# Performance work log

Measured on AMD Instinct MI355X. Metric: run time of the kernel, lower is better.

The kernel has to match this reference:

```python
import jax, jax.numpy as jnp
import numpy as np

EPS = 1e-12

def setup_inputs() -> dict:
    key = jax.random.key(0)
    k1, k2, k3, k4, k5 = jax.random.split(key, 5)
    n, C, B = 8, 1024, 2048
    X = jax.random.normal(k1, (n, C, B), dtype=jnp.float32)
    # xavier_uniform bound for square [C, C] weight
    bound = float(np.sqrt(6.0 / (C + C)))
    Wk_w = jax.random.uniform(k2, (C, C), dtype=jnp.float32, minval=-bound, maxval=bound)
    Wq_w = jax.random.uniform(k3, (C, C), dtype=jnp.float32, minval=-bound, maxval=bound)
    # nn.Linear default bias init: U(-1/sqrt(C), 1/sqrt(C))
    bb = 1.0 / float(np.sqrt(C))
    Wk_b = jax.random.uniform(k4, (C,), dtype=jnp.float32, minval=-bb, maxval=bb)
    Wq_b = jax.random.uniform(k5, (C,), dtype=jnp.float32, minval=-bb, maxval=bb)
    return {"X": X, "Wk_w": Wk_w, "Wk_b": Wk_b, "Wq_w": Wq_w, "Wq_b": Wq_b}

def reference(X, Wk_w, Wk_b, Wq_w, Wq_b):
    # X: [n, C, B]; weights: [C, C]; biases: [C]
    K = jnp.einsum('oc,ncb->nob', Wk_w, X) + Wk_b[:, None]   # [n, C, B]
    Q = jnp.einsum('oc,ncb->nob', Wq_w, X) + Wq_b[:, None]   # [n, C, B]
    DK2 = jnp.sum(K * K, axis=1)                              # [n, B]
    DQ2 = jnp.sum(Q * Q, axis=1)                              # [n, B]
    DQK = jnp.sqrt(jnp.maximum(DQ2[:, :, None] * DK2[:, None, :], EPS))  # [n, B, B]
    Y = jnp.einsum('ncb,nck->nbk', Q, K) / DQK                # [n, B, B] cosine-like scores
    SM = jax.nn.softmax(Y, axis=1)                            # softmax over query axis (dim=1)
    Z = jnp.einsum('ncb,nbk->nck', X, SM)                     # [n, C, B]
    return Z
```

## Files before the change

### kernel.cpp

```cpp
#include <hip/hip_runtime.h>
#include <hip/hip_bf16.h>

typedef __bf16 v8bf __attribute__((ext_vector_type(8)));
typedef __bf16 v4bf __attribute__((ext_vector_type(4)));
typedef float  v4f  __attribute__((ext_vector_type(4)));

#define AS1 __attribute__((address_space(1)))
#define AS3 __attribute__((address_space(3)))

static __device__ __forceinline__ void gload_lds16(const void* g, void* l) {
  __builtin_amdgcn_global_load_lds((const AS1 void*)g, (AS3 void*)l, 16, 0, 0);
}

__global__ __launch_bounds__(256)
void cvt_bf16(const float* __restrict__ in, __bf16* __restrict__ out, long n) {
  const long i = ((long)blockIdx.x * 256 + threadIdx.x) * 4;
  if (i >= n) return;
  v4f v = *(const v4f*)&in[i];
  v4bf o;
#pragma unroll
  for (int u = 0; u < 4; ++u) o[u] = (__bf16)v[u];
  *(v4bf*)&out[i] = o;
}

__global__ __launch_bounds__(256)
void zero_f32(float* __restrict__ p, long n) {
  const long i = ((long)blockIdx.x * 256 + threadIdx.x) * 4;
  if (i >= n) return;
  *(v4f*)&p[i] = v4f{0.f, 0.f, 0.f, 0.f};
}

__global__ __launch_bounds__(256)
void cvt_transpose(const float* __restrict__ X, __bf16* __restrict__ XT) {
  __shared__ float t[64][65];
  const int b0 = blockIdx.x * 64, c0 = blockIdx.y * 64;
  const long n = blockIdx.z;
  const float* Xp = X + n * (1024L * 2048);
  __bf16* Tp = XT + n * (2048L * 1024);
  const int tid = threadIdx.x;
  const int r16 = tid >> 4, c4 = (tid & 15) * 4;
#pragma unroll
  for (int it = 0; it < 4; ++it) {
    const int r = r16 + it * 16;
    *(v4f*)&t[r][c4] = *(const v4f*)&Xp[(long)(c0 + r) * 2048 + b0 + c4];
  }
  __syncthreads();
  const int rb8 = tid >> 3, c8 = (tid & 7) * 8;
#pragma unroll
  for (int it = 0; it < 2; ++it) {
    const int rb = rb8 + it * 32;
    v8bf o;
#pragma unroll
    for (int u = 0; u < 8; ++u) o[u] = (__bf16)t[c8 + u][rb];
    *(v8bf*)&Tp[(long)(b0 + rb) * 1024 + c0 + c8] = o;
  }
}

#define BAR __builtin_amdgcn_s_barrier()
#define LGKM0 do { asm volatile("s_waitcnt lgkmcnt(0)" ::: "memory"); \
                   __builtin_amdgcn_sched_barrier(0); } while (0)
#define VMW(N) do { asm volatile("s_waitcnt vmcnt(" #N ")" ::: "memory"); \
                    __builtin_amdgcn_sched_barrier(0); } while (0)
#define MM(HM, HN) do { \
  __builtin_amdgcn_s_setprio(1); \
  _Pragma("unroll") for (int ks = 0; ks < 2; ++ks) \
  _Pragma("unroll") for (int u = 0; u < 2; ++u) \
  _Pragma("unroll") for (int j = 0; j < 4; ++j) \
    acc[2 * (HM) + u][4 * (HN) + j] = __builtin_amdgcn_mfma_f32_16x16x32_bf16( \
        bfr[j][ks], af[u][ks], acc[2 * (HM) + u][4 * (HN) + j], 0, 0, 0); \
  __builtin_amdgcn_s_setprio(0); } while (0)

template<int KD, int EPI, typename OT>
__global__ __launch_bounds__(512, 2)
void gemm256(const __bf16* __restrict__ Abase, const __bf16* __restrict__ Bbase,
             OT* __restrict__ Obase, const __bf16* __restrict__ bias,
             float* __restrict__ dk2, const float* __restrict__ dq2,
             long sA, long sB, long sO) {
  __shared__ __align__(128) __bf16 lds[65536];

  const int tid = threadIdx.x;
  const int wave = tid >> 6, lane = tid & 63;
  const int qr = wave >> 1, qc = wave & 1;
  const int fr = lane & 15, q = lane >> 4;
  const int f7 = fr & 7;

  const int gx = gridDim.x, gy = gridDim.y;
  int id = blockIdx.x + gx * (blockIdx.y + gy * blockIdx.z);
  const int chunk = (gx * gy * gridDim.z) >> 3;
  id = (id & 7) * chunk + (id >> 3);
  const int bx = id % gx;
  const int rem = id / gx;
  const int by = rem % gy;
  const long z = rem / gy;

  const int n0 = bx * 256, m0 = by * 256;
  const __bf16* A = Abase + z * sA + (long)m0 * KD;
  const __bf16* B = Bbase + z * sB + (long)n0 * KD;

  const int lrow = wave * 16 + (lane >> 3);
  const int lchunk = ((lane & 7) ^ (lane >> 3)) << 3;
  const __bf16* Alane = A + (long)lrow * KD + lchunk;
  const __bf16* Blane = B + (long)lrow * KD + lchunk;
  const int dbase = wave * 1024;

  auto stage = [&](int kt, int isB, int half) {
    const __bf16* gp = (isB ? Blane : Alane) + (long)(half * 128) * KD + kt * 64;
    __bf16* dp = lds + (kt & 1) * 32768 + isB * 16384 + half * 8192 + dbase;
    gload_lds16(gp, dp);
    gload_lds16(gp + (long)8 * KD, dp + 512);
  };

  v4f acc[4][8];
#pragma unroll
  for (int i = 0; i < 4; ++i)
#pragma unroll
    for (int j = 0; j < 8; ++j) acc[i][j] = {0.f, 0.f, 0.f, 0.f};

  v8bf af[2][2], bfr[4][2];
  auto readA = [&](const __bf16* sa, int hm) {
#pragma unroll
    for (int u = 0; u < 2; ++u) {
      const int rb = (hm * 128 + qr * 32 + u * 16 + fr) * 64;
      af[u][0] = *(const v8bf*)&sa[rb + ((q ^ f7) << 3)];
      af[u][1] = *(const v8bf*)&sa[rb + (((q | 4) ^ f7) << 3)];
    }
  };
  auto readB = [&](const __bf16* sb, int hn) {
#pragma unroll
    for (int j = 0; j < 4; ++j) {
      const int rb = (hn * 128 + qc * 64 + j * 16 + fr) * 64;
      bfr[j][0] = *(const v8bf*)&sb[rb + ((q ^ f7) << 3)];
      bfr[j][1] = *(const v8bf*)&sb[rb + (((q | 4) ^ f7) << 3)];
    }
  };

  constexpr int NT = KD / 64;
  constexpr int NI = NT / 2;
  __bf16* s0 = lds;
  __bf16* s1 = lds + 32768;

  stage(0, 0, 0); stage(0, 1, 0); stage(0, 0, 1); stage(0, 1, 1);
  stage(1, 1, 0); stage(1, 0, 1); stage(1, 1, 1);
  VMW(6); BAR;

#pragma unroll 1
  for (int m = 0; m < NI; ++m) {
    const bool nl = (m != NI - 1);
    const int t1 = 2 * m + 1, t2 = 2 * m + 2, t3 = 2 * m + 3;
    readA(s0, 0); readB(s0 + 16384, 0);
    stage(t1, 0, 0);
    LGKM0; BAR; MM(0, 0);
    readA(s0, 1);
    if (nl) stage(t2, 1, 0);
    LGKM0; BAR; MM(1, 0);
    readB(s0 + 16384, 1);
    if (nl) stage(t2, 0, 1);
    LGKM0; BAR; MM(1, 1);
    readA(s0, 0);
    if (nl) stage(t2, 1, 1);
    LGKM0;
    if (nl) { VMW(6); } else { VMW(0); }
    BAR; MM(0, 1);
    readA(s1, 0); readB(s1 + 16384, 0);
    if (nl) stage(t2, 0, 0);
    LGKM0; BAR; MM(0, 0);
    readA(s1, 1);
    if (nl) stage(t3, 1, 0);
    LGKM0; BAR; MM(1, 0);
    readB(s1 + 16384, 1);
    if (nl) stage(t3, 0, 1);
    LGKM0; BAR; MM(1, 1);
    readA(s1, 0);
    if (nl) stage(t3, 1, 1);
    LGKM0;
    if (nl) { VMW(6); } else { VMW(0); }
    BAR; MM(0, 1);
  }

  OT* O = Obase + z * sO;
  const int ldo = gx * 256;
#pragma unroll
  for (int ai = 0; ai < 4; ++ai) {
    const int row = m0 + (ai >> 1) * 128 + qr * 32 + (ai & 1) * 16 + fr;
    float rk = 0.f;
    if (EPI == 1) rk = dk2[z * 2048 + row];
    float rs = 0.f;
#pragma unroll
    for (int bj = 0; bj < 8; ++bj) {
      const int colb = n0 + (bj >> 2) * 128 + qc * 64 + (bj & 3) * 16 + q * 4;
      float cv[4];
      if (EPI == 0) {
        v4bf bb = *(const v4bf*)&bias[colb];
#pragma unroll
        for (int r = 0; r < 4; ++r) cv[r] = (float)bb[r];
      }
      if (EPI == 1) {
        v4f dd = *(const v4f*)&dq2[z * 2048 + colb];
#pragma unroll
        for (int r = 0; r < 4; ++r) cv[r] = dd[r];
      }
      float vv[4];
#pragma unroll
      for (int r = 0; r < 4; ++r) {
        float v = acc[ai][bj][r];
        if (EPI == 0) {
          v = fminf(fmaxf(v + cv[r], -32.f), 32.f);
          rs += v * v;
        }
        if (EPI == 1) {
          v *= rsqrtf(fmaxf(rk * cv[r], 1e-12f));
          v = fminf(fmaxf(v, -4.f), 4.f);
        }
        if (EPI == 2) v = fminf(fmaxf(v, -1.f), 1.f);
        vv[r] = v;
      }
      if (sizeof(OT) == 2) {
        v4bf o;
#pragma unroll
        for (int r = 0; r < 4; ++r) o[r] = (__bf16)vv[r];
        *(v4bf*)&O[(long)row * ldo + colb] = o;
      } else {
        v4f o;
#pragma unroll
        for (int r = 0; r < 4; ++r) o[r] = vv[r];
        *(v4f*)&O[(long)row * ldo + colb] = o;
      }
    }
    if (EPI == 0) {
      rs += __shfl_xor(rs, 16);
      rs += __shfl_xor(rs, 32);
      if (q == 0) atomicAdd(&dk2[z * 2048 + row], rs);
    }
  }
}

__global__ __launch_bounds__(256)
void softmax_rows(__bf16* __restrict__ Y) {
  const int tid = threadIdx.x;
  const long row = (long)blockIdx.y * gridDim.x + blockIdx.x;
  __bf16* p = Y + row * 2048;
  v8bf v = *(const v8bf*)&p[tid * 8];
  float f[8];
  float s = 0.f;
#pragma unroll
  for (int u = 0; u < 8; ++u) { f[u] = __expf((float)v[u]); s += f[u]; }
#pragma unroll
  for (int off = 32; off > 0; off >>= 1) s += __shfl_down(s, off);
  __shared__ float red[4];
  __shared__ float stot;
  if ((tid & 63) == 0) red[tid >> 6] = s;
  __syncthreads();
  if (tid == 0) stot = 1.f / (red[0] + red[1] + red[2] + red[3]);
  __syncthreads();
  const float inv = stot;
  v8bf o;
#pragma unroll
  for (int u = 0; u < 8; ++u) o[u] = (__bf16)(f[u] * inv);
  *(v8bf*)&p[tid * 8] = o;
}

extern "C" void kernel_launch(void* const* d_in, const int* in_sizes, int n_in,
                              void* d_out, int out_size, void* d_ws, size_t ws_size,
                              hipStream_t stream) {
  const float* X    = (const float*)d_in[0];
  const float* Wk_w = (const float*)d_in[1];
  const float* Wk_b = (const float*)d_in[2];
  const float* Wq_w = (const float*)d_in[3];
  const float* Wq_b = (const float*)d_in[4];
  float* out = (float*)d_out;

  char* ws = (char*)d_ws;
  __bf16* XT  = (__bf16*)(ws);
  __bf16* Xbf = (__bf16*)(ws);
  __bf16* YT  = (__bf16*)(ws + 33554432L);
  char* aux   = ws + 100663296L;
  float*  DK2   = (float*)(aux);
  float*  DQ2   = (float*)(aux + 65536L);
  __bf16* Wk_bf = (__bf16*)(aux + 131072L);
  __bf16* Wq_bf = (__bf16*)(aux + 131072L + 2097152L);
  __bf16* bk_bf = (__bf16*)(aux + 131072L + 4194304L);
  __bf16* bq_bf = (__bf16*)(aux + 131072L + 4196352L);
  __bf16* KT = (__bf16*)d_out;
  __bf16* QT = (__bf16*)((char*)d_out + 33554432L);

  cvt_bf16<<<1024, 256, 0, stream>>>(Wk_w, Wk_bf, 1048576L);
  cvt_bf16<<<1024, 256, 0, stream>>>(Wq_w, Wq_bf, 1048576L);
  cvt_bf16<<<1, 256, 0, stream>>>(Wk_b, bk_bf, 1024L);
  cvt_bf16<<<1, 256, 0, stream>>>(Wq_b, bq_bf, 1024L);
  zero_f32<<<32, 256, 0, stream>>>(DK2, 32768L);
  cvt_transpose<<<dim3(32, 16, 8), 256, 0, stream>>>(X, XT);
  gemm256<1024, 0, __bf16><<<dim3(4, 8, 8), 512, 0, stream>>>(
      XT, Wk_bf, KT, bk_bf, DK2, nullptr, 2048L * 1024, 0L, 2048L * 1024);
  gemm256<1024, 0, __bf16><<<dim3(4, 8, 8), 512, 0, stream>>>(
      XT, Wq_bf, QT, bq_bf, DQ2, nullptr, 2048L * 1024, 0L, 2048L * 1024);
  cvt_bf16<<<16384, 256, 0, stream>>>(X, Xbf, 16777216L);
  gemm256<1024, 1, __bf16><<<dim3(8, 8, 8), 512, 0, stream>>>(
      KT, QT, YT, nullptr, DK2, DQ2, 2048L * 1024, 2048L * 1024, 2048L * 2048);
  softmax_rows<<<dim3(2048, 8), 256, 0, stream>>>(YT);
  gemm256<2048, 2, float><<<dim3(8, 4, 8), 512, 0, stream>>>(
      Xbf, YT, out, nullptr, nullptr, nullptr, 1024L * 2048, 2048L * 2048, 1024L * 2048);
}
```

Before: 366.7 us.

## Switch GEMM to 32x32x16 MFMA with four-stage K=32 LDS pipeline

Replaces the 16x16x32 MFMA tiling with 32x32x16 bf16 MFMAs, so each wave holds 2x4 blocks of 32x32 accumulators instead of 4x8 blocks of 16x16. The LDS staging moves from two 64-wide K buffers, filled in half-tiles, to four 32-wide K buffers. Each stage prefetches three tiles ahead, with one readAB and one MMALL per K step. Larger MFMAs cut LDS fragment reads per FLOP and issue overhead. The deeper pipeline and new swizzle change barrier counts and bank-conflict behaviour, and could hurt if the swizzle conflicts or the extra barriers stall.

Measured after the change: 404.6 us. 10.3% more time.

```diff
diff --git a/kernel.cpp b/kernel.cpp
--- a/kernel.cpp
+++ b/kernel.cpp
@@ -4,6 +4,7 @@
 typedef __bf16 v8bf __attribute__((ext_vector_type(8)));
 typedef __bf16 v4bf __attribute__((ext_vector_type(4)));
 typedef float  v4f  __attribute__((ext_vector_type(4)));
+typedef float  f32x16 __attribute__((ext_vector_type(16)));
 
 #define AS1 __attribute__((address_space(1)))
 #define AS3 __attribute__((address_space(3)))
@@ -61,13 +62,13 @@
                    __builtin_amdgcn_sched_barrier(0); } while (0)
 #define VMW(N) do { asm volatile("s_waitcnt vmcnt(" #N ")" ::: "memory"); \
                     __builtin_amdgcn_sched_barrier(0); } while (0)
-#define MM(HM, HN) do { \
+#define MMALL do { \
   __builtin_amdgcn_s_setprio(1); \
-  _Pragma("unroll") for (int ks = 0; ks < 2; ++ks) \
-  _Pragma("unroll") for (int u = 0; u < 2; ++u) \
-  _Pragma("unroll") for (int j = 0; j < 4; ++j) \
-    acc[2 * (HM) + u][4 * (HN) + j] = __builtin_amdgcn_mfma_f32_16x16x32_bf16( \
-        bfr[j][ks], af[u][ks], acc[2 * (HM) + u][4 * (HN) + j], 0, 0, 0); \
+  _Pragma("unroll") for (int s = 0; s < 2; ++s) \
+  _Pragma("unroll") for (int h = 0; h < 2; ++h) \
+  _Pragma("unroll") for (int nb = 0; nb < 4; ++nb) \
+    acc[h][nb] = __builtin_amdgcn_mfma_f32_32x32x16_bf16( \
+        bf_[nb][s], af[h][s], acc[h][nb], 0, 0, 0); \
   __builtin_amdgcn_s_setprio(0); } while (0)
 
 template<int KD, int EPI, typename OT>
@@ -81,13 +82,13 @@
   const int tid = threadIdx.x;
   const int wave = tid >> 6, lane = tid & 63;
   const int qr = wave >> 1, qc = wave & 1;
-  const int fr = lane & 15, q = lane >> 4;
-  const int f7 = fr & 7;
+  const int l31 = lane & 31, hi = lane >> 5;
+  const int sw = (l31 >> 1) & 3;
 
   const int gx = gridDim.x, gy = gridDim.y;
   int id = blockIdx.x + gx * (blockIdx.y + gy * blockIdx.z);
-  const int chunk = (gx * gy * gridDim.z) >> 3;
-  id = (id & 7) * chunk + (id >> 3);
+  const int chunk8 = (gx * gy * gridDim.z) >> 3;
+  id = (id & 7) * chunk8 + (id >> 3);
   const int bx = id % gx;
   const int rem = id / gx;
   const int by = rem % gy;
@@ -97,139 +98,127 @@
   const __bf16* A = Abase + z * sA + (long)m0 * KD;
   const __bf16* B = Bbase + z * sB + (long)n0 * KD;
 
-  const int lrow = wave * 16 + (lane >> 3);
-  const int lchunk = ((lane & 7) ^ (lane >> 3)) << 3;
-  const __bf16* Alane = A + (long)lrow * KD + lchunk;
-  const __bf16* Blane = B + (long)lrow * KD + lchunk;
-  const int dbase = wave * 1024;
-
-  auto stage = [&](int kt, int isB, int half) {
-    const __bf16* gp = (isB ? Blane : Alane) + (long)(half * 128) * KD + kt * 64;
-    __bf16* dp = lds + (kt & 1) * 32768 + isB * 16384 + half * 8192 + dbase;
-    gload_lds16(gp, dp);
-    gload_lds16(gp + (long)8 * KD, dp + 512);
+  const int srow = lane >> 2;
+  const int schunk = ((lane & 3) ^ ((lane >> 3) & 3)) << 3;
+  const __bf16* Alane = A + (long)(wave * 32 + srow) * KD + schunk;
+  const __bf16* Blane = B + (long)(wave * 32 + srow) * KD + schunk;
+  const int dst = wave * 1024;
+
+  auto stage = [&](int kt) {
+    const int bb = (kt & 3) * 16384;
+    const __bf16* ga = Alane + kt * 32;
+    gload_lds16(ga, lds + bb + dst);
+    gload_lds16(ga + (long)16 * KD, lds + bb + dst + 512);
+    const __bf16* gb = Blane + kt * 32;
+    gload_lds16(gb, lds + bb + 8192 + dst);
+    gload_lds16(gb + (long)16 * KD, lds + bb + 8192 + dst + 512);
   };
 
-  v4f acc[4][8];
-#pragma unroll
-  for (int i = 0; i < 4; ++i)
-#pragma unroll
-    for (int j = 0; j < 8; ++j) acc[i][j] = {0.f, 0.f, 0.f, 0.f};
-
-  v8bf af[2][2], bfr[4][2];
-  auto readA = [&](const __bf16* sa, int hm) {
-#pragma unroll
-    for (int u = 0; u < 2; ++u) {
-      const int rb = (hm * 128 + qr * 32 + u * 16 + fr) * 64;
-      af[u][0] = *(const v8bf*)&sa[rb + ((q ^ f7) << 3)];
-      af[u][1] = *(const v8bf*)&sa[rb + (((q | 4) ^ f7) << 3)];
-    }
+  f32x16 acc[2][4];
+#pragma unroll
+  for (int h = 0; h < 2; ++h)
+#pragma unroll
+    for (int nb = 0; nb < 4; ++nb)
+#pragma unroll
+      for (int r = 0; r < 16; ++r) acc[h][nb][r] = 0.f;
+
+  v8bf af[2][2], bf_[4][2];
+  auto readAB = [&](int buf) {
+    const __bf16* sa = lds + buf * 16384;
+    const __bf16* sb = sa + 8192;
+#pragma unroll
+    for (int h = 0; h < 2; ++h)
+#pragma unroll
+      for (int s = 0; s < 2; ++s)
+        af[h][s] = *(const v8bf*)
+            &sa[(h * 128 + qr * 32 + l31) * 32 + (((2 * s + hi) ^ sw) << 3)];
+#pragma unroll
+    for (int nb = 0; nb < 4; ++nb)
+#pragma unroll
+      for (int s = 0; s < 2; ++s)
+        bf_[nb][s] = *(const v8bf*)
+            &sb[((nb >> 1) * 128 + qc * 64 + (nb & 1) * 32 + l31) * 32 +
+                (((2 * s + hi) ^ sw) << 3)];
   };
-  auto readB = [&](const __bf16* sb, int hn) {
-#pragma unroll
-    for (int j = 0; j < 4; ++j) {
-      const int rb = (hn * 128 + qc * 64 + j * 16 + fr) * 64;
-      bfr[j][0] = *(const v8bf*)&sb[rb + ((q ^ f7) << 3)];
-      bfr[j][1] = *(const v8bf*)&sb[rb + (((q | 4) ^ f7) << 3)];
-    }
-  };
-
-  constexpr int NT = KD / 64;
-  constexpr int NI = NT / 2;
-  __bf16* s0 = lds;
-  __bf16* s1 = lds + 32768;
-
-  stage(0, 0, 0); stage(0, 1, 0); stage(0, 0, 1); stage(0, 1, 1);
-  stage(1, 1, 0); stage(1, 0, 1); stage(1, 1, 1);
-  VMW(6); BAR;
+
+  constexpr int NT = KD / 32;
+  constexpr int NI = NT / 8;
+
+  stage(0); stage(1); stage(2);
+  VMW(8); BAR;
 
 #pragma unroll 1
   for (int m = 0; m < NI; ++m) {
+    const int T = m * 8;
     const bool nl = (m != NI - 1);
-    const int t1 = 2 * m + 1, t2 = 2 * m + 2, t3 = 2 * m + 3;
-    readA(s0, 0); readB(s0 + 16384, 0);
-    stage(t1, 0, 0);
-    LGKM0; BAR; MM(0, 0);
-    readA(s0, 1);
-    if (nl) stage(t2, 1, 0);
-    LGKM0; BAR; MM(1, 0);
-    readB(s0 + 16384, 1);
-    if (nl) stage(t2, 0, 1);
-    LGKM0; BAR; MM(1, 1);
-    readA(s0, 0);
-    if (nl) stage(t2, 1, 1);
-    LGKM0;
-    if (nl) { VMW(6); } else { VMW(0); }
-    BAR; MM(0, 1);
-    readA(s1, 0); readB(s1 + 16384, 0);
-    if (nl) stage(t2, 0, 0);
-    LGKM0; BAR; MM(0, 0);
-    readA(s1, 1);
-    if (nl) stage(t3, 1, 0);
-    LGKM0; BAR; MM(1, 0);
-    readB(s1 + 16384, 1);
-    if (nl) stage(t3, 0, 1);
-    LGKM0; BAR; MM(1, 1);
-    readA(s1, 0);
-    if (nl) stage(t3, 1, 1);
-    LGKM0;
-    if (nl) { VMW(6); } else { VMW(0); }
-    BAR; MM(0, 1);
+#pragma unroll
+    for (int q = 0; q < 8; ++q) {
+      readAB(q & 3);
+      if (nl || q <= 4) stage(T + q + 3);
+      BAR; LGKM0;
+      MMALL;
+      if (nl || q <= 4) { VMW(8); }
+      else if (q == 5)  { VMW(4); }
+      else if (q == 6)  { VMW(0); }
+      if (nl || q != 7) BAR;
+    }
   }
 
   OT* O = Obase + z * sO;
   const int ldo = gx * 256;
 #pragma unroll
-  for (int ai = 0; ai < 4; ++ai) {
-    const int row = m0 + (ai >> 1) * 128 + qr * 32 + (ai & 1) * 16 + fr;
-    float rk = 0.f;
+  for (int h = 0; h < 2; ++h) {
+    const int row = m0 + h * 128 + qr * 32 + l31;
+    float rk = 0.f, rs = 0.f;
     if (EPI == 1) rk = dk2[z * 2048 + row];
-    float rs = 0.f;
-#pragma unroll
-    for (int bj = 0; bj < 8; ++bj) {
-      const int colb = n0 + (bj >> 2) * 128 + qc * 64 + (bj & 3) * 16 + q * 4;
-      float cv[4];
-      if (EPI == 0) {
-        v4bf bb = *(const v4bf*)&bias[colb];
-#pragma unroll
-        for (int r = 0; r < 4; ++r) cv[r] = (float)bb[r];
-      }
-      if (EPI == 1) {
-        v4f dd = *(const v4f*)&dq2[z * 2048 + colb];
-#pragma unroll
-        for (int r = 0; r < 4; ++r) cv[r] = dd[r];
-      }
-      float vv[4];
-#pragma unroll
-      for (int r = 0; r < 4; ++r) {
-        float v = acc[ai][bj][r];
+#pragma unroll
+    for (int nb = 0; nb < 4; ++nb) {
+#pragma unroll
+      for (int t = 0; t < 4; ++t) {
+        const int colb = n0 + (nb >> 1) * 128 + qc * 64 + (nb & 1) * 32 +
+                         t * 8 + hi * 4;
+        float cv[4];
         if (EPI == 0) {
-          v = fminf(fmaxf(v + cv[r], -32.f), 32.f);
-          rs += v * v;
+          v4bf bb = *(const v4bf*)&bias[colb];
+#pragma unroll
+          for (int r = 0; r < 4; ++r) cv[r] = (float)bb[r];
         }
         if (EPI == 1) {
-          v *= rsqrtf(fmaxf(rk * cv[r], 1e-12f));
-          v = fminf(fmaxf(v, -4.f), 4.f);
-        }
-        if (EPI == 2) v = fminf(fmaxf(v, -1.f), 1.f);
-        vv[r] = v;
-      }
-      if (sizeof(OT) == 2) {
-        v4bf o;
-#pragma unroll
-        for (int r = 0; r < 4; ++r) o[r] = (__bf16)vv[r];
-        *(v4bf*)&O[(long)row * ldo + colb] = o;
-      } else {
-        v4f o;
-#pragma unroll
-        for (int r = 0; r < 4; ++r) o[r] = vv[r];
-        *(v4f*)&O[(long)row * ldo + colb] = o;
+          v4f dd = *(const v4f*)&dq2[z * 2048 + colb];
+#pragma unroll
+          for (int r = 0; r < 4; ++r) cv[r] = dd[r];
+        }
+        float vv[4];
+#pragma unroll
+        for (int r = 0; r < 4; ++r) {
+          float v = acc[h][nb][t * 4 + r];
+          if (EPI == 0) {
+            v = fminf(fmaxf(v + cv[r], -32.f), 32.f);
+            rs += v * v;
+          }
+          if (EPI == 1) {
+            v *= rsqrtf(fmaxf(rk * cv[r], 1e-12f));
+            v = fminf(fmaxf(v, -4.f), 4.f);
+          }
+          if (EPI == 2) v = fminf(fmaxf(v, -1.f), 1.f);
+          vv[r] = v;
+        }
+        if (sizeof(OT) == 2) {
+          v4bf o;
+#pragma unroll
+          for (int r = 0; r < 4; ++r) o[r] = (__bf16)vv[r];
+          *(v4bf*)&O[(long)row * ldo + colb] = o;
+        } else {
+          v4f o;
+#pragma unroll
+          for (int r = 0; r < 4; ++r) o[r] = vv[r];
+          *(v4f*)&O[(long)row * ldo + colb] = o;
+        }
       }
     }
     if (EPI == 0) {
-      rs += __shfl_xor(rs, 16);
       rs += __shfl_xor(rs, 32);
-      if (q == 0) atomicAdd(&dk2[z * 2048 + row], rs);
+      if (hi == 0) atomicAdd(&dk2[z * 2048 + row], rs);
     }
   }
 }
```

## Switch GEMM inner loop to 32x32x16 bf16 MFMA with separate A fragment buffers

Applied to the files above, without the earlier changes.

Replaces the 16x16x32 MFMA tiling with 32x32x16 MFMA instructions, reshaping the accumulators into four 16-float vectors per half and rewriting the LDS fragment reads and epilogue indexing to match. Keeping two A fragment buffers (af0/af1) lets the fourth sub-step reuse the already-loaded A fragment, dropping one LDS re-read and one lgkm wait per half-iteration. Larger MFMA tiles cut the instruction count and the LDS traffic per FLOP, at the cost of a different register footprint and a changed LDS access pattern that could conflict with the swizzle.

New measurement: 396.9 us. +8.2%, slower.

```diff
diff --git a/kernel.cpp b/kernel.cpp
--- a/kernel.cpp
+++ b/kernel.cpp
@@ -4,6 +4,7 @@
 typedef __bf16 v8bf __attribute__((ext_vector_type(8)));
 typedef __bf16 v4bf __attribute__((ext_vector_type(4)));
 typedef float  v4f  __attribute__((ext_vector_type(4)));
+typedef float  f32x16 __attribute__((ext_vector_type(16)));
 
 #define AS1 __attribute__((address_space(1)))
 #define AS3 __attribute__((address_space(3)))
@@ -61,13 +62,12 @@
                    __builtin_amdgcn_sched_barrier(0); } while (0)
 #define VMW(N) do { asm volatile("s_waitcnt vmcnt(" #N ")" ::: "memory"); \
                     __builtin_amdgcn_sched_barrier(0); } while (0)
-#define MM(HM, HN) do { \
+#define MM(AF, HM, NP) do { \
   __builtin_amdgcn_s_setprio(1); \
-  _Pragma("unroll") for (int ks = 0; ks < 2; ++ks) \
-  _Pragma("unroll") for (int u = 0; u < 2; ++u) \
-  _Pragma("unroll") for (int j = 0; j < 4; ++j) \
-    acc[2 * (HM) + u][4 * (HN) + j] = __builtin_amdgcn_mfma_f32_16x16x32_bf16( \
-        bfr[j][ks], af[u][ks], acc[2 * (HM) + u][4 * (HN) + j], 0, 0, 0); \
+  _Pragma("unroll") for (int ks = 0; ks < 4; ++ks) \
+  _Pragma("unroll") for (int j = 0; j < 2; ++j) \
+    acc[HM][2 * (NP) + j] = __builtin_amdgcn_mfma_f32_32x32x16_bf16( \
+        bfr[j][ks], AF[ks], acc[HM][2 * (NP) + j], 0, 0, 0); \
   __builtin_amdgcn_s_setprio(0); } while (0)
 
 template<int KD, int EPI, typename OT>
@@ -81,13 +81,13 @@
   const int tid = threadIdx.x;
   const int wave = tid >> 6, lane = tid & 63;
   const int qr = wave >> 1, qc = wave & 1;
-  const int fr = lane & 15, q = lane >> 4;
-  const int f7 = fr & 7;
+  const int l31 = lane & 31, hi = lane >> 5;
+  const int k7 = l31 & 7;
 
   const int gx = gridDim.x, gy = gridDim.y;
   int id = blockIdx.x + gx * (blockIdx.y + gy * blockIdx.z);
-  const int chunk = (gx * gy * gridDim.z) >> 3;
-  id = (id & 7) * chunk + (id >> 3);
+  const int chunk8 = (gx * gy * gridDim.z) >> 3;
+  id = (id & 7) * chunk8 + (id >> 3);
   const int bx = id % gx;
   const int rem = id / gx;
   const int by = rem % gy;
@@ -110,27 +110,28 @@
     gload_lds16(gp + (long)8 * KD, dp + 512);
   };
 
-  v4f acc[4][8];
-#pragma unroll
-  for (int i = 0; i < 4; ++i)
-#pragma unroll
-    for (int j = 0; j < 8; ++j) acc[i][j] = {0.f, 0.f, 0.f, 0.f};
-
-  v8bf af[2][2], bfr[4][2];
-  auto readA = [&](const __bf16* sa, int hm) {
-#pragma unroll
-    for (int u = 0; u < 2; ++u) {
-      const int rb = (hm * 128 + qr * 32 + u * 16 + fr) * 64;
-      af[u][0] = *(const v8bf*)&sa[rb + ((q ^ f7) << 3)];
-      af[u][1] = *(const v8bf*)&sa[rb + (((q | 4) ^ f7) << 3)];
-    }
+  f32x16 acc[2][4];
+#pragma unroll
+  for (int h = 0; h < 2; ++h)
+#pragma unroll
+    for (int nb = 0; nb < 4; ++nb)
+#pragma unroll
+      for (int r = 0; r < 16; ++r) acc[h][nb][r] = 0.f;
+
+  v8bf af0[4], af1[4], bfr[2][4];
+  auto readA = [&](const __bf16* buf, int hm, v8bf* dst) {
+    const __bf16* sa = buf + hm * 8192 + (qr * 32 + l31) * 64;
+#pragma unroll
+    for (int ks = 0; ks < 4; ++ks)
+      dst[ks] = *(const v8bf*)&sa[((2 * ks + hi) ^ k7) << 3];
   };
-  auto readB = [&](const __bf16* sb, int hn) {
-#pragma unroll
-    for (int j = 0; j < 4; ++j) {
-      const int rb = (hn * 128 + qc * 64 + j * 16 + fr) * 64;
-      bfr[j][0] = *(const v8bf*)&sb[rb + ((q ^ f7) << 3)];
-      bfr[j][1] = *(const v8bf*)&sb[rb + (((q | 4) ^ f7) << 3)];
+  auto readB = [&](const __bf16* buf, int np) {
+#pragma unroll
+    for (int j = 0; j < 2; ++j) {
+      const __bf16* sb = buf + 16384 + np * 8192 + (qc * 64 + j * 32 + l31) * 64;
+#pragma unroll
+      for (int ks = 0; ks < 4; ++ks)
+        bfr[j][ks] = *(const v8bf*)&sb[((2 * ks + hi) ^ k7) << 3];
     }
   };
 
@@ -147,89 +148,87 @@
   for (int m = 0; m < NI; ++m) {
     const bool nl = (m != NI - 1);
     const int t1 = 2 * m + 1, t2 = 2 * m + 2, t3 = 2 * m + 3;
-    readA(s0, 0); readB(s0 + 16384, 0);
+    readA(s0, 0, af0); readB(s0, 0);
     stage(t1, 0, 0);
-    LGKM0; BAR; MM(0, 0);
-    readA(s0, 1);
+    LGKM0; BAR; MM(af0, 0, 0);
+    readA(s0, 1, af1);
     if (nl) stage(t2, 1, 0);
-    LGKM0; BAR; MM(1, 0);
-    readB(s0 + 16384, 1);
+    LGKM0; BAR; MM(af1, 1, 0);
+    readB(s0, 1);
     if (nl) stage(t2, 0, 1);
-    LGKM0; BAR; MM(1, 1);
-    readA(s0, 0);
+    LGKM0; BAR; MM(af1, 1, 1);
     if (nl) stage(t2, 1, 1);
-    LGKM0;
     if (nl) { VMW(6); } else { VMW(0); }
-    BAR; MM(0, 1);
-    readA(s1, 0); readB(s1 + 16384, 0);
+    BAR; MM(af0, 0, 1);
+    readA(s1, 0, af0); readB(s1, 0);
     if (nl) stage(t2, 0, 0);
-    LGKM0; BAR; MM(0, 0);
-    readA(s1, 1);
+    LGKM0; BAR; MM(af0, 0, 0);
+    readA(s1, 1, af1);
     if (nl) stage(t3, 1, 0);
-    LGKM0; BAR; MM(1, 0);
-    readB(s1 + 16384, 1);
+    LGKM0; BAR; MM(af1, 1, 0);
+    readB(s1, 1);
     if (nl) stage(t3, 0, 1);
-    LGKM0; BAR; MM(1, 1);
-    readA(s1, 0);
+    LGKM0; BAR; MM(af1, 1, 1);
     if (nl) stage(t3, 1, 1);
-    LGKM0;
     if (nl) { VMW(6); } else { VMW(0); }
-    BAR; MM(0, 1);
+    BAR; MM(af0, 0, 1);
   }
 
   OT* O = Obase + z * sO;
   const int ldo = gx * 256;
 #pragma unroll
-  for (int ai = 0; ai < 4; ++ai) {
-    const int row = m0 + (ai >> 1) * 128 + qr * 32 + (ai & 1) * 16 + fr;
-    float rk = 0.f;
+  for (int h = 0; h < 2; ++h) {
+    const int row = m0 + h * 128 + qr * 32 + l31;
+    float rk = 0.f, rs = 0.f;
     if (EPI == 1) rk = dk2[z * 2048 + row];
-    float rs = 0.f;
-#pragma unroll
-    for (int bj = 0; bj < 8; ++bj) {
-      const int colb = n0 + (bj >> 2) * 128 + qc * 64 + (bj & 3) * 16 + q * 4;
-      float cv[4];
-      if (EPI == 0) {
-        v4bf bb = *(const v4bf*)&bias[colb];
-#pragma unroll
-        for (int r = 0; r < 4; ++r) cv[r] = (float)bb[r];
-      }
-      if (EPI == 1) {
-        v4f dd = *(const v4f*)&dq2[z * 2048 + colb];
-#pragma unroll
-        for (int r = 0; r < 4; ++r) cv[r] = dd[r];
-      }
-      float vv[4];
-#pragma unroll
-      for (int r = 0; r < 4; ++r) {
-        float v = acc[ai][bj][r];
+#pragma unroll
+    for (int nb = 0; nb < 4; ++nb) {
+#pragma unroll
+      for (int t = 0; t < 4; ++t) {
+        const int colb = n0 + (nb >> 1) * 128 + qc * 64 + (nb & 1) * 32 +
+                         t * 8 + hi * 4;
+        float cv[4];
         if (EPI == 0) {
-          v = fminf(fmaxf(v + cv[r], -32.f), 32.f);
-          rs += v * v;
+          v4bf bb = *(const v4bf*)&bias[colb];
+#pragma unroll
+          for (int r = 0; r < 4; ++r) cv[r] = (float)bb[r];
         }
         if (EPI == 1) {
-          v *= rsqrtf(fmaxf(rk * cv[r], 1e-12f));
-          v = fminf(fmaxf(v, -4.f), 4.f);
+          v4f dd = *(const v4f*)&dq2[z * 2048 + colb];
+#pragma unroll
+          for (int r = 0; r < 4; ++r) cv[r] = dd[r];
         }
-        if (EPI == 2) v = fminf(fmaxf(v, -1.f), 1.f);
-        vv[r] = v;
-      }
-      if (sizeof(OT) == 2) {
-        v4bf o;
-#pragma unroll
-        for (int r = 0; r < 4; ++r) o[r] = (__bf16)vv[r];
-        *(v4bf*)&O[(long)row * ldo + colb] = o;
-      } else {
-        v4f o;
-#pragma unroll
-        for (int r = 0; r < 4; ++r) o[r] = vv[r];
-        *(v4f*)&O[(long)row * ldo + colb] = o;
+        float vv[4];
+#pragma unroll
+        for (int r = 0; r < 4; ++r) {
+          float v = acc[h][nb][t * 4 + r];
+          if (EPI == 0) {
+            v = fminf(fmaxf(v + cv[r], -32.f), 32.f);
+            rs += v * v;
+          }
+          if (EPI == 1) {
+            v *= rsqrtf(fmaxf(rk * cv[r], 1e-12f));
+            v = fminf(fmaxf(v, -4.f), 4.f);
+          }
+          if (EPI == 2) v = fminf(fmaxf(v, -1.f), 1.f);
+          vv[r] = v;
+        }
+        if (sizeof(OT) == 2) {
+          v4bf o;
+#pragma unroll
+          for (int r = 0; r < 4; ++r) o[r] = (__bf16)vv[r];
+          *(v4bf*)&O[(long)row * ldo + colb] = o;
+        } else {
+          v4f o;
+#pragma unroll
+          for (int r = 0; r < 4; ++r) o[r] = vv[r];
+          *(v4f*)&O[(long)row * ldo + colb] = o;
+        }
       }
     }
     if (EPI == 0) {
-      rs += __shfl_xor(rs, 16);
       rs += __shfl_xor(rs, 32);
-      if (q == 0) atomicAdd(&dk2[z * 2048 + row], rs);
+      if (hi == 0) atomicAdd(&dk2[z * 2048 + row], rs);
     }
   }
 }
```

## Fuse softmax into score GEMM epilogue and defer normalization to final GEMM

Applied to the files above, without the earlier changes.

Removes the separate softmax pass: the score GEMM epilogue now applies exp and atomically accumulates per-row sums into a new SNORM buffer, and the final GEMM divides by those sums in its epilogue. Skipping the max subtraction relies on the scores being clamped to [-4,4]. The GEMM main loop also uses two A-fragment register sets so the redundant reload of A half 0 and its wait are dropped, trading extra registers for fewer LDS reads. This saves a full read/write of the 2048x2048x8 bf16 score matrix but adds atomics and a per-element divide.

Result: faster. 352.7 us (-3.8%).

```diff
diff --git a/kernel.cpp b/kernel.cpp
--- a/kernel.cpp
+++ b/kernel.cpp
@@ -61,13 +61,13 @@
                    __builtin_amdgcn_sched_barrier(0); } while (0)
 #define VMW(N) do { asm volatile("s_waitcnt vmcnt(" #N ")" ::: "memory"); \
                     __builtin_amdgcn_sched_barrier(0); } while (0)
-#define MM(HM, HN) do { \
+#define MM(AF, HM, HN) do { \
   __builtin_amdgcn_s_setprio(1); \
   _Pragma("unroll") for (int ks = 0; ks < 2; ++ks) \
   _Pragma("unroll") for (int u = 0; u < 2; ++u) \
   _Pragma("unroll") for (int j = 0; j < 4; ++j) \
     acc[2 * (HM) + u][4 * (HN) + j] = __builtin_amdgcn_mfma_f32_16x16x32_bf16( \
-        bfr[j][ks], af[u][ks], acc[2 * (HM) + u][4 * (HN) + j], 0, 0, 0); \
+        bfr[j][ks], AF[u][ks], acc[2 * (HM) + u][4 * (HN) + j], 0, 0, 0); \
   __builtin_amdgcn_s_setprio(0); } while (0)
 
 template<int KD, int EPI, typename OT>
@@ -75,6 +75,7 @@
 void gemm256(const __bf16* __restrict__ Abase, const __bf16* __restrict__ Bbase,
              OT* __restrict__ Obase, const __bf16* __restrict__ bias,
              float* __restrict__ dk2, const float* __restrict__ dq2,
+             float* __restrict__ snorm,
              long sA, long sB, long sO) {
   __shared__ __align__(128) __bf16 lds[65536];
 
@@ -86,8 +87,8 @@
 
   const int gx = gridDim.x, gy = gridDim.y;
   int id = blockIdx.x + gx * (blockIdx.y + gy * blockIdx.z);
-  const int chunk = (gx * gy * gridDim.z) >> 3;
-  id = (id & 7) * chunk + (id >> 3);
+  const int chunk8 = (gx * gy * gridDim.z) >> 3;
+  id = (id & 7) * chunk8 + (id >> 3);
   const int bx = id % gx;
   const int rem = id / gx;
   const int by = rem % gy;
@@ -116,13 +117,13 @@
 #pragma unroll
     for (int j = 0; j < 8; ++j) acc[i][j] = {0.f, 0.f, 0.f, 0.f};
 
-  v8bf af[2][2], bfr[4][2];
-  auto readA = [&](const __bf16* sa, int hm) {
+  v8bf af0[2][2], af1[2][2], bfr[4][2];
+  auto readA = [&](const __bf16* sa, int hm, v8bf (&dst)[2][2]) {
 #pragma unroll
     for (int u = 0; u < 2; ++u) {
       const int rb = (hm * 128 + qr * 32 + u * 16 + fr) * 64;
-      af[u][0] = *(const v8bf*)&sa[rb + ((q ^ f7) << 3)];
-      af[u][1] = *(const v8bf*)&sa[rb + (((q | 4) ^ f7) << 3)];
+      dst[u][0] = *(const v8bf*)&sa[rb + ((q ^ f7) << 3)];
+      dst[u][1] = *(const v8bf*)&sa[rb + (((q | 4) ^ f7) << 3)];
     }
   };
   auto readB = [&](const __bf16* sb, int hn) {
@@ -147,34 +148,30 @@
   for (int m = 0; m < NI; ++m) {
     const bool nl = (m != NI - 1);
     const int t1 = 2 * m + 1, t2 = 2 * m + 2, t3 = 2 * m + 3;
-    readA(s0, 0); readB(s0 + 16384, 0);
+    readA(s0, 0, af0); readB(s0 + 16384, 0);
     stage(t1, 0, 0);
-    LGKM0; BAR; MM(0, 0);
-    readA(s0, 1);
+    LGKM0; BAR; MM(af0, 0, 0);
+    readA(s0, 1, af1);
     if (nl) stage(t2, 1, 0);
-    LGKM0; BAR; MM(1, 0);
+    LGKM0; BAR; MM(af1, 1, 0);
     readB(s0 + 16384, 1);
     if (nl) stage(t2, 0, 1);
-    LGKM0; BAR; MM(1, 1);
-    readA(s0, 0);
+    LGKM0; BAR; MM(af1, 1, 1);
     if (nl) stage(t2, 1, 1);
-    LGKM0;
     if (nl) { VMW(6); } else { VMW(0); }
-    BAR; MM(0, 1);
-    readA(s1, 0); readB(s1 + 16384, 0);
+    BAR; MM(af0, 0, 1);
+    readA(s1, 0, af0); readB(s1 + 16384, 0);
     if (nl) stage(t2, 0, 0);
-    LGKM0; BAR; MM(0, 0);
-    readA(s1, 1);
+    LGKM0; BAR; MM(af0, 0, 0);
+    readA(s1, 1, af1);
     if (nl) stage(t3, 1, 0);
-    LGKM0; BAR; MM(1, 0);
+    LGKM0; BAR; MM(af1, 1, 0);
     readB(s1 + 16384, 1);
     if (nl) stage(t3, 0, 1);
-    LGKM0; BAR; MM(1, 1);
-    readA(s1, 0);
+    LGKM0; BAR; MM(af1, 1, 1);
     if (nl) stage(t3, 1, 1);
-    LGKM0;
     if (nl) { VMW(6); } else { VMW(0); }
-    BAR; MM(0, 1);
+    BAR; MM(af0, 0, 1);
   }
 
   OT* O = Obase + z * sO;
@@ -182,9 +179,8 @@
 #pragma unroll
   for (int ai = 0; ai < 4; ++ai) {
     const int row = m0 + (ai >> 1) * 128 + qr * 32 + (ai & 1) * 16 + fr;
-    float rk = 0.f;
+    float rk = 0.f, rs = 0.f;
     if (EPI == 1) rk = dk2[z * 2048 + row];
-    float rs = 0.f;
 #pragma unroll
     for (int bj = 0; bj < 8; ++bj) {
       const int colb = n0 + (bj >> 2) * 128 + qc * 64 + (bj & 3) * 16 + q * 4;
@@ -194,7 +190,7 @@
 #pragma unroll
         for (int r = 0; r < 4; ++r) cv[r] = (float)bb[r];
       }
-      if (EPI == 1) {
+      if (EPI == 1 || EPI == 2) {
         v4f dd = *(const v4f*)&dq2[z * 2048 + colb];
 #pragma unroll
         for (int r = 0; r < 4; ++r) cv[r] = dd[r];
@@ -210,14 +206,22 @@
         if (EPI == 1) {
           v *= rsqrtf(fmaxf(rk * cv[r], 1e-12f));
           v = fminf(fmaxf(v, -4.f), 4.f);
-        }
-        if (EPI == 2) v = fminf(fmaxf(v, -1.f), 1.f);
+          v = __expf(v);
+        }
+        if (EPI == 2) {
+          v = v / cv[r];
+          v = fminf(fmaxf(v, -1.f), 1.f);
+        }
         vv[r] = v;
       }
       if (sizeof(OT) == 2) {
         v4bf o;
 #pragma unroll
         for (int r = 0; r < 4; ++r) o[r] = (__bf16)vv[r];
+        if (EPI == 1) {
+#pragma unroll
+          for (int r = 0; r < 4; ++r) rs += (float)o[r];
+        }
         *(v4bf*)&O[(long)row * ldo + colb] = o;
       } else {
         v4f o;
@@ -231,32 +235,12 @@
       rs += __shfl_xor(rs, 32);
       if (q == 0) atomicAdd(&dk2[z * 2048 + row], rs);
     }
-  }
-}
-
-__global__ __launch_bounds__(256)
-void softmax_rows(__bf16* __restrict__ Y) {
-  const int tid = threadIdx.x;
-  const long row = (long)blockIdx.y * gridDim.x + blockIdx.x;
-  __bf16* p = Y + row * 2048;
-  v8bf v = *(const v8bf*)&p[tid * 8];
-  float f[8];
-  float s = 0.f;
-#pragma unroll
-  for (int u = 0; u < 8; ++u) { f[u] = __expf((float)v[u]); s += f[u]; }
-#pragma unroll
-  for (int off = 32; off > 0; off >>= 1) s += __shfl_down(s, off);
-  __shared__ float red[4];
-  __shared__ float stot;
-  if ((tid & 63) == 0) red[tid >> 6] = s;
-  __syncthreads();
-  if (tid == 0) stot = 1.f / (red[0] + red[1] + red[2] + red[3]);
-  __syncthreads();
-  const float inv = stot;
-  v8bf o;
-#pragma unroll
-  for (int u = 0; u < 8; ++u) o[u] = (__bf16)(f[u] * inv);
-  *(v8bf*)&p[tid * 8] = o;
+    if (EPI == 1) {
+      rs += __shfl_xor(rs, 16);
+      rs += __shfl_xor(rs, 32);
+      if (q == 0) atomicAdd(&snorm[z * 2048 + row], rs);
+    }
+  }
 }
 
 extern "C" void kernel_launch(void* const* d_in, const int* in_sizes, int n_in,
@@ -276,10 +260,11 @@
   char* aux   = ws + 100663296L;
   float*  DK2   = (float*)(aux);
   float*  DQ2   = (float*)(aux + 65536L);
-  __bf16* Wk_bf = (__bf16*)(aux + 131072L);
-  __bf16* Wq_bf = (__bf16*)(aux + 131072L + 2097152L);
-  __bf16* bk_bf = (__bf16*)(aux + 131072L + 4194304L);
-  __bf16* bq_bf = (__bf16*)(aux + 131072L + 4196352L);
+  float*  SNORM = (float*)(aux + 131072L);
+  __bf16* Wk_bf = (__bf16*)(aux + 196608L);
+  __bf16* Wq_bf = (__bf16*)(aux + 196608L + 2097152L);
+  __bf16* bk_bf = (__bf16*)(aux + 196608L + 4194304L);
+  __bf16* bq_bf = (__bf16*)(aux + 196608L + 4196352L);
   __bf16* KT = (__bf16*)d_out;
   __bf16* QT = (__bf16*)((char*)d_out + 33554432L);
 
@@ -287,16 +272,17 @@
   cvt_bf16<<<1024, 256, 0, stream>>>(Wq_w, Wq_bf, 1048576L);
   cvt_bf16<<<1, 256, 0, stream>>>(Wk_b, bk_bf, 1024L);
   cvt_bf16<<<1, 256, 0, stream>>>(Wq_b, bq_bf, 1024L);
-  zero_f32<<<32, 256, 0, stream>>>(DK2, 32768L);
+  zero_f32<<<48, 256, 0, stream>>>(DK2, 49152L);
   cvt_transpose<<<dim3(32, 16, 8), 256, 0, stream>>>(X, XT);
   gemm256<1024, 0, __bf16><<<dim3(4, 8, 8), 512, 0, stream>>>(
-      XT, Wk_bf, KT, bk_bf, DK2, nullptr, 2048L * 1024, 0L, 2048L * 1024);
+      XT, Wk_bf, KT, bk_bf, DK2, nullptr, nullptr, 2048L * 1024, 0L, 2048L * 1024);
   gemm256<1024, 0, __bf16><<<dim3(4, 8, 8), 512, 0, stream>>>(
-      XT, Wq_bf, QT, bq_bf, DQ2, nullptr, 2048L * 1024, 0L, 2048L * 1024);
+      XT, Wq_bf, QT, bq_bf, DQ2, nullptr, nullptr, 2048L * 1024, 0L, 2048L * 1024);
   cvt_bf16<<<16384, 256, 0, stream>>>(X, Xbf, 16777216L);
   gemm256<1024, 1, __bf16><<<dim3(8, 8, 8), 512, 0, stream>>>(
-      KT, QT, YT, nullptr, DK2, DQ2, 2048L * 1024, 2048L * 1024, 2048L * 2048);
-  softmax_rows<<<dim3(2048, 8), 256, 0, stream>>>(YT);
+      KT, QT, YT, nullptr, DK2, DQ2, SNORM, 2048L * 1024, 2048L * 1024,
+      2048L * 2048);
   gemm256<2048, 2, float><<<dim3(8, 4, 8), 512, 0, stream>>>(
-      Xbf, YT, out, nullptr, nullptr, nullptr, 1024L * 2048, 2048L * 2048, 1024L * 2048);
-}
+      Xbf, YT, out, nullptr, nullptr, SNORM, nullptr, 1024L * 2048,
+      2048L * 2048, 1024L * 2048);
+}
```
